# Optimization experiments

Measured on AMD Instinct MI355X. Metric: run time of the kernel, lower is better.

## Reference

```python
import jax, jax.numpy as jnp
import numpy as np
from jax import lax

T, B, NI, NH = 512, 64, 512, 512
SIGMA = 0.01


def _rnn_scan(inputs, W_xh, W_hh, b_h, h0):
    # inputs: [T, B, NI]; precompute input projection as one big GEMM
    xw = jnp.einsum('tbi,ih->tbh', inputs, W_xh)  # [T, B, NH]

    def step(h, x):
        h = jnp.tanh(x + h @ W_hh + b_h)
        return h, h

    hT, hs = lax.scan(step, h0, xw)
    return hs, hT  # hs: [T, B, NH]


def setup_inputs() -> dict:
    key = jax.random.key(0)
    ks = jax.random.split(key, 5)
    inputs = jax.random.normal(ks[0], (T, B, NI), dtype=jnp.float32)
    W_xh_f = jax.random.normal(ks[1], (NI, NH), dtype=jnp.float32) * SIGMA
    W_hh_f = jax.random.normal(ks[2], (NH, NH), dtype=jnp.float32) * SIGMA
    b_h_f = jnp.zeros((NH,), dtype=jnp.float32)
    W_xh_b = jax.random.normal(ks[3], (NI, NH), dtype=jnp.float32) * SIGMA
    W_hh_b = jax.random.normal(ks[4], (NH, NH), dtype=jnp.float32) * SIGMA
    b_h_b = jnp.zeros((NH,), dtype=jnp.float32)
    return {"inputs": inputs, "W_xh_f": W_xh_f, "W_hh_f": W_hh_f, "b_h_f": b_h_f,
            "W_xh_b": W_xh_b, "W_hh_b": W_hh_b, "b_h_b": b_h_b}


def reference(inputs, W_xh_f, W_hh_f, b_h_f, W_xh_b, W_hh_b, b_h_b):
    h0 = jnp.zeros((inputs.shape[1], NH), dtype=inputs.dtype)
    f_outs, f_H = _rnn_scan(inputs, W_xh_f, W_hh_f, b_h_f, h0)
    b_outs_rev, b_H = _rnn_scan(inputs[::-1], W_xh_b, W_hh_b, b_h_b, h0)
    b_outs = b_outs_rev[::-1]  # align backward outputs with forward time order
    outputs = jnp.concatenate([f_outs, b_outs], axis=-1)  # [T, B, 2*NH]
    return outputs, f_H, b_H
```

## Files before the change

### kernel.cpp

```cpp
#include <hip/hip_runtime.h>
#include <hip/hip_bf16.h>


typedef __attribute__((ext_vector_type(8))) short short8;
typedef __attribute__((ext_vector_type(4))) float f32x4;
typedef __attribute__((ext_vector_type(4))) int   i32x4;

static __device__ __forceinline__ unsigned short f2bf(float f) {
  unsigned int u = __builtin_bit_cast(unsigned int, f);
  u = (u + 0x7fffu + ((u >> 16) & 1u)) >> 16;
  return (unsigned short)u;
}
static __device__ __forceinline__ float bf2f(unsigned short s) {
  return __builtin_bit_cast(float, ((unsigned int)s) << 16);
}
static __device__ __forceinline__ float tanh_cheap(float x) {
  float t = x * 2.8853900817779268f;
  float e;
  asm("v_exp_f32 %0, %1" : "=v"(e) : "v"(t));
  float den = e + 1.0f;
  float r;
  asm("v_rcp_f32 %0, %1" : "=v"(r) : "v"(den));
  return __builtin_fmaf(-2.0f, r, 1.0f);
}
static __device__ __forceinline__ void lds_barrier() {
  __builtin_amdgcn_sched_barrier(0);
  asm volatile("s_waitcnt lgkmcnt(0)" ::: "memory");
  __builtin_amdgcn_s_barrier();
  __builtin_amdgcn_sched_barrier(0);
}
static __device__ __forceinline__ unsigned int cvt_pk_bf16(float a, float b) {
  unsigned int d;
  asm("v_cvt_pk_bf16_f32 %0, %1, %2" : "=v"(d) : "v"(a), "v"(b));
  return d;
}

__global__ __launch_bounds__(256, 2) void xw_gemm(
    const float* __restrict__ inp,
    const float* __restrict__ Wf,
    const float* __restrict__ Wb,
    const float* __restrict__ bhf,
    const float* __restrict__ bhb,
    unsigned short* __restrict__ xwpf,
    unsigned short* __restrict__ xwpb) {
  __shared__ unsigned short As[64 * 40];
  __shared__ unsigned short Bfs[64 * 40];
  __shared__ unsigned short Bbs[64 * 40];
  const int tid = threadIdx.x;
  const int w = tid >> 6, l = tid & 63;
  const int lr = l & 15, lg = l >> 4;
  const int rbase = blockIdx.x * 64;
  const int nbase = blockIdx.y * 64;

  f32x4 accf[4], accb[4];
#pragma unroll
  for (int tn = 0; tn < 4; ++tn) { accf[tn] = (f32x4){0,0,0,0}; accb[tn] = (f32x4){0,0,0,0}; }

  for (int i = 0; i < 16; ++i) {
    const int k0 = i * 32;
    __syncthreads();
#pragma unroll
    for (int e = 0; e < 2; ++e) {
      int lin4 = tid + e * 256;
      int r = lin4 >> 3, c4 = (lin4 & 7) * 4;
      float4 v = *reinterpret_cast<const float4*>(&inp[(rbase + r) * 512 + k0 + c4]);
      unsigned short* dst = &As[r * 40 + c4];
      dst[0] = f2bf(v.x); dst[1] = f2bf(v.y); dst[2] = f2bf(v.z); dst[3] = f2bf(v.w);
    }
#pragma unroll
    for (int e = 0; e < 2; ++e) {
      int lin4 = tid + e * 256;
      int r = lin4 >> 4, c4 = (lin4 & 15) * 4;
      float4 vf = *reinterpret_cast<const float4*>(&Wf[(k0 + r) * 512 + nbase + c4]);
      float4 vb = *reinterpret_cast<const float4*>(&Wb[(k0 + r) * 512 + nbase + c4]);
      Bfs[(c4 + 0) * 40 + r] = f2bf(vf.x);
      Bfs[(c4 + 1) * 40 + r] = f2bf(vf.y);
      Bfs[(c4 + 2) * 40 + r] = f2bf(vf.z);
      Bfs[(c4 + 3) * 40 + r] = f2bf(vf.w);
      Bbs[(c4 + 0) * 40 + r] = f2bf(vb.x);
      Bbs[(c4 + 1) * 40 + r] = f2bf(vb.y);
      Bbs[(c4 + 2) * 40 + r] = f2bf(vb.z);
      Bbs[(c4 + 3) * 40 + r] = f2bf(vb.w);
    }
    __syncthreads();
    const int ar = w * 16 + lr;
    const int kg = lg * 8;
    short8 a = *reinterpret_cast<const short8*>(&As[ar * 40 + kg]);
#pragma unroll
    for (int tn = 0; tn < 4; ++tn) {
      const int bc = tn * 16 + lr;
      short8 bf = *reinterpret_cast<const short8*>(&Bfs[bc * 40 + kg]);
      short8 bb = *reinterpret_cast<const short8*>(&Bbs[bc * 40 + kg]);
      accf[tn] = __builtin_amdgcn_mfma_f32_16x16x32_bf16(a, bf, accf[tn], 0, 0, 0);
      accb[tn] = __builtin_amdgcn_mfma_f32_16x16x32_bf16(a, bb, accb[tn], 0, 0, 0);
    }
  }
  unsigned long long* pf = reinterpret_cast<unsigned long long*>(xwpf);
  unsigned long long* pb = reinterpret_cast<unsigned long long*>(xwpb);
  const int b64 = (((int)blockIdx.x * 4 + w) * 8 + (int)blockIdx.y) * 256 + (lg * 16 + lr) * 4;
#pragma unroll
  for (int tn = 0; tn < 4; ++tn) {
    const int colb = nbase + tn * 16 + lr;
    const float bfv = bhf[colb], bbv = bhb[colb];
    unsigned long long vf =
        (unsigned long long)cvt_pk_bf16(accf[tn][0] + bfv, accf[tn][1] + bfv)
      | ((unsigned long long)cvt_pk_bf16(accf[tn][2] + bfv, accf[tn][3] + bfv) << 32);
    unsigned long long vb =
        (unsigned long long)cvt_pk_bf16(accb[tn][0] + bbv, accb[tn][1] + bbv)
      | ((unsigned long long)cvt_pk_bf16(accb[tn][2] + bbv, accb[tn][3] + bbv) << 32);
    pf[b64 + tn] = vf;
    pb[b64 + tn] = vb;
  }
}

__global__ __launch_bounds__(512, 2) void birnn_scan(
    const float* __restrict__ Whf, const float* __restrict__ Whb,
    unsigned short* __restrict__ xwpf, unsigned short* __restrict__ xwpb,
    float* __restrict__ out) {
  const int bid = blockIdx.x;
  const int d  = bid >> 2;
  const int rg = bid & 3;
  const int tid = threadIdx.x;
  const int w = tid >> 6, l = tid & 63;
  const int lr = l & 15, lg = l >> 4;
  const int cbase = w * 64;
  const int rbase = rg * 16;

  const float* Wh = d ? Whb : Whf;
  unsigned short* xwp = d ? xwpb : xwpf;

  __shared__ __align__(16) signed char hq[2][8192];

  const float sW = 127.0f / 0.06f;
  i32x4 wq[4][8];
#pragma unroll
  for (int n = 0; n < 4; ++n) {
    const int col = cbase + n * 16 + lr;
#pragma unroll
    for (int kk = 0; kk < 8; ++kk) {
      i32x4 v;
#pragma unroll
      for (int dw = 0; dw < 4; ++dw) {
        unsigned int pack = 0;
#pragma unroll
        for (int jj = 0; jj < 4; ++jj) {
          const int k = kk * 64 + lg * 16 + dw * 4 + jj;
          float wv = Wh[k * 512 + col] * sW;
          wv = fminf(fmaxf(wv, -127.f), 127.f);
          int q = (int)rintf(wv);
          pack |= ((unsigned int)(q & 0xff)) << (8 * jj);
        }
        v[dw] = (int)pack;
      }
      wq[n][kk] = v;
    }
  }
  const float inv_s = 1.0f / (127.0f * sW);

  short8 xA0, xA1, xB0, xB1;
  {
    const int t0 = d ? 511 : 0;
    const unsigned short* p = xwp + (((t0 * 4 + rg) * 8 + w) << 10) + (l << 4);
    xA0 = *reinterpret_cast<const short8*>(p);
    xA1 = *reinterpret_cast<const short8*>(p + 8);
  }
  {
    const int t1 = d ? 510 : 1;
    const unsigned short* p = xwp + (((t1 * 4 + rg) * 8 + w) << 10) + (l << 4);
    xB0 = *reinterpret_cast<const short8*>(p);
    xB1 = *reinterpret_cast<const short8*>(p + 8);
  }

  uint4 HP0, HP1;

#define XV_EXTRACT(XLO, XHI)                                                  \
    float xv[4][4];                                                           \
    _Pragma("unroll") for (int n = 0; n < 2; ++n)                             \
      _Pragma("unroll") for (int q = 0; q < 4; ++q) {                         \
        xv[n][q]     = bf2f((unsigned short)XLO[n * 4 + q]);                  \
        xv[n + 2][q] = bf2f((unsigned short)XHI[n * 4 + q]);                  \
      }

#define EPI(N, ACC, U0, U1, FINAL_)                                           \
  {                                                                           \
    float h0_ = tanh_cheap(fmaf((float)(ACC)[0], inv_s, xv[N][0]));           \
    float h1_ = tanh_cheap(fmaf((float)(ACC)[1], inv_s, xv[N][1]));           \
    float h2_ = tanh_cheap(fmaf((float)(ACC)[2], inv_s, xv[N][2]));           \
    float h3_ = tanh_cheap(fmaf((float)(ACC)[3], inv_s, xv[N][3]));           \
    signed char* hd_ = &hq[buf_][(w * 4 + (N)) * 256 + lg * 64 + lr];         \
    hd_[0]  = (signed char)(int)rintf(h0_ * 127.f);                           \
    hd_[16] = (signed char)(int)rintf(h1_ * 127.f);                           \
    hd_[32] = (signed char)(int)rintf(h2_ * 127.f);                           \
    hd_[48] = (signed char)(int)rintf(h3_ * 127.f);                           \
    U0 = cvt_pk_bf16(h0_, h1_);                                               \
    U1 = cvt_pk_bf16(h2_, h3_);                                               \
    if (FINAL_) {                                                             \
      float* fo_ = out + 33554432 + d * 32768 + (rbase + lg * 4) * 512 +      \
                   cbase + (N) * 16 + lr;                                     \
      fo_[0] = h0_; fo_[512] = h1_; fo_[1024] = h2_; fo_[1536] = h3_;         \
    }                                                                         \
  }

#define CHAIN(ACC, N)                                                         \
  ACC = __builtin_amdgcn_mfma_i32_16x16x64_i8(a0, wq[N][0], ACC, 0, 0, 0);    \
  ACC = __builtin_amdgcn_mfma_i32_16x16x64_i8(a1, wq[N][1], ACC, 0, 0, 0);    \
  ACC = __builtin_amdgcn_mfma_i32_16x16x64_i8(a2, wq[N][2], ACC, 0, 0, 0);    \
  ACC = __builtin_amdgcn_mfma_i32_16x16x64_i8(a3, wq[N][3], ACC, 0, 0, 0);    \
  ACC = __builtin_amdgcn_mfma_i32_16x16x64_i8(a4, wq[N][4], ACC, 0, 0, 0);    \
  ACC = __builtin_amdgcn_mfma_i32_16x16x64_i8(a5, wq[N][5], ACC, 0, 0, 0);    \
  ACC = __builtin_amdgcn_mfma_i32_16x16x64_i8(a6, wq[N][6], ACC, 0, 0, 0);    \
  ACC = __builtin_amdgcn_mfma_i32_16x16x64_i8(a7, wq[N][7], ACC, 0, 0, 0);

#define STEP(S, XLO, XHI, FINAL_)                                             \
  do {                                                                        \
    const int s_ = (S);                                                       \
    const int t_ = d ? (511 - s_) : s_;                                       \
    const int buf_ = s_ & 1;                                                  \
    const signed char* hb_ = &hq[(s_ - 1) & 1][lg * 256 + lr * 16];           \
    i32x4 a0 = *(const i32x4*)(hb_ + 0);                                      \
    i32x4 a1 = *(const i32x4*)(hb_ + 1024);                                   \
    i32x4 a2 = *(const i32x4*)(hb_ + 2048);                                   \
    i32x4 a3 = *(const i32x4*)(hb_ + 3072);                                   \
    i32x4 a4 = *(const i32x4*)(hb_ + 4096);                                   \
    i32x4 a5 = *(const i32x4*)(hb_ + 5120);                                   \
    i32x4 a6 = *(const i32x4*)(hb_ + 6144);                                   \
    i32x4 a7 = *(const i32x4*)(hb_ + 7168);                                   \
    XV_EXTRACT(XLO, XHI);                                                     \
    {                                                                         \
      const int tp2_ = d ? (t_ - 2) : (t_ + 2);                               \
      const unsigned short* p_ =                                              \
          xwp + (((tp2_ * 4 + rg) * 8 + w) << 10) + (l << 4);                 \
      XLO = *reinterpret_cast<const short8*>(p_);                             \
      XHI = *reinterpret_cast<const short8*>(p_ + 8);                         \
    }                                                                         \
    {              \
      const int tp_ = d ? (t_ + 1) : (t_ - 1);                                \
      unsigned short* pw_ = xwp + (((tp_ * 4 + rg) * 8 + w) << 10) + (l << 4);\
      *reinterpret_cast<uint4*>(pw_) = HP0;                                   \
      *reinterpret_cast<uint4*>(pw_ + 8) = HP1;                               \
    }                                                                         \
    i32x4 acc0 = (i32x4){0,0,0,0}, acc1 = (i32x4){0,0,0,0};                   \
    i32x4 acc2 = (i32x4){0,0,0,0}, acc3 = (i32x4){0,0,0,0};                   \
    CHAIN(acc0, 0);                                                           \
    CHAIN(acc1, 1);                                                           \
    EPI(0, acc0, HP0.x, HP0.y, FINAL_);                                       \
    CHAIN(acc2, 2);                                                           \
    EPI(1, acc1, HP0.z, HP0.w, FINAL_);                                       \
    CHAIN(acc3, 3);                                                           \
    EPI(2, acc2, HP1.x, HP1.y, FINAL_);                                       \
    EPI(3, acc3, HP1.z, HP1.w, FINAL_);                                       \
    lds_barrier();                                                            \
  } while (0)

  {
    const int t_ = d ? 511 : 0;
    const int buf_ = 0;
    XV_EXTRACT(xA0, xA1);
    {
      const int tp2_ = d ? (t_ - 2) : (t_ + 2);
      const unsigned short* p_ = xwp + (((tp2_ * 4 + rg) * 8 + w) << 10) + (l << 4);
      xA0 = *reinterpret_cast<const short8*>(p_);
      xA1 = *reinterpret_cast<const short8*>(p_ + 8);
    }
    i32x4 z_ = (i32x4){0, 0, 0, 0};
    EPI(0, z_, HP0.x, HP0.y, 0);
    EPI(1, z_, HP0.z, HP0.w, 0);
    EPI(2, z_, HP1.x, HP1.y, 0);
    EPI(3, z_, HP1.z, HP1.w, 0);
    lds_barrier();
  }

  for (int ss = 0; ss < 255; ++ss) {
    STEP(1 + 2 * ss, xB0, xB1, 0);
    STEP(2 + 2 * ss, xA0, xA1, 0);
  }
  STEP(511, xB0, xB1, 1);

  {
    const int tl_ = d ? 0 : 511;
    unsigned short* pw_ = xwp + (((tl_ * 4 + rg) * 8 + w) << 10) + (l << 4);
    *reinterpret_cast<uint4*>(pw_) = HP0;
    *reinterpret_cast<uint4*>(pw_ + 8) = HP1;
  }
#undef STEP
#undef CHAIN
#undef EPI
#undef XV_EXTRACT
}

__global__ __launch_bounds__(1024) void expand_out(
    const unsigned short* __restrict__ xwpf,
    const unsigned short* __restrict__ xwpb,
    float* __restrict__ out) {
  const int g = blockIdx.x * 1024 + threadIdx.x;
  const int flat = g * 4;
  const int row = flat >> 10;
  const int c   = flat & 1023;
  const int t = row >> 6, b = row & 63;
  const int d = c >> 9, col = c & 511;
  const unsigned short* buf = d ? xwpb : xwpf;
  const int lr0 = col & 15;
  const int base = ((((t * 4 + (b >> 4)) * 8 + (col >> 6)) << 10) +
                    ((b >> 2) & 3) * 256 + ((col >> 4) & 3) * 4 + (b & 3));
  float4 v;
  v.x = bf2f(buf[base + (lr0 + 0) * 16]);
  v.y = bf2f(buf[base + (lr0 + 1) * 16]);
  v.z = bf2f(buf[base + (lr0 + 2) * 16]);
  v.w = bf2f(buf[base + (lr0 + 3) * 16]);
  *reinterpret_cast<float4*>(out + flat) = v;
}

extern "C" void kernel_launch(void* const* d_in, const int* in_sizes, int n_in,
                              void* d_out, int out_size, void* d_ws, size_t ws_size,
                              hipStream_t stream) {
  (void)in_sizes; (void)n_in; (void)out_size; (void)ws_size;
  const float* inputs = (const float*)d_in[0];
  const float* W_xh_f = (const float*)d_in[1];
  const float* W_hh_f = (const float*)d_in[2];
  const float* b_h_f  = (const float*)d_in[3];
  const float* W_xh_b = (const float*)d_in[4];
  const float* W_hh_b = (const float*)d_in[5];
  const float* b_h_b  = (const float*)d_in[6];

  unsigned short* xwpf = (unsigned short*)d_ws;
  unsigned short* xwpb = xwpf + 16777216 + 65536;

  dim3 g1(512, 8), b1(256);
  xw_gemm<<<g1, b1, 0, stream>>>(inputs, W_xh_f, W_xh_b, b_h_f, b_h_b, xwpf, xwpb);

  birnn_scan<<<dim3(8), dim3(512), 0, stream>>>(
      W_hh_f, W_hh_b, xwpf, xwpb, (float*)d_out);

  expand_out<<<dim3(8192), dim3(1024), 0, stream>>>(xwpf, xwpb, (float*)d_out);
}
```

Baseline: 889.8 us.

## Split recurrent scan across 16 waves with two interleaved MFMA chains each

Doubles the scan block to 1024 threads so each wave owns 32 hidden columns instead of 64. Each wave now runs two independent int8 MFMA accumulator chains, interleaved, under raised wave priority, which shortens the serial per-step critical path. The xw/h workspace layout changes to match in the GEMM writer, the scan and expand_out. The cost is more waves contending at the per-step barrier and only one wave per SIMD group of four, possibly leaving latency less hidden.

```diff
diff --git a/kernel.cpp b/kernel.cpp
--- a/kernel.cpp
+++ b/kernel.cpp
@@ -97,7 +97,8 @@
   }
   unsigned long long* pf = reinterpret_cast<unsigned long long*>(xwpf);
   unsigned long long* pb = reinterpret_cast<unsigned long long*>(xwpb);
-  const int b64 = (((int)blockIdx.x * 4 + w) * 8 + (int)blockIdx.y) * 256 + (lg * 16 + lr) * 4;
+  const int b64 = (((int)blockIdx.x * 4 + w) * 16 + (int)blockIdx.y * 2) * 128 +
+                  (lg * 16 + lr) * 2;
 #pragma unroll
   for (int tn = 0; tn < 4; ++tn) {
     const int colb = nbase + tn * 16 + lr;
@@ -108,12 +109,12 @@
     unsigned long long vb =
         (unsigned long long)cvt_pk_bf16(accb[tn][0] + bbv, accb[tn][1] + bbv)
       | ((unsigned long long)cvt_pk_bf16(accb[tn][2] + bbv, accb[tn][3] + bbv) << 32);
-    pf[b64 + tn] = vf;
-    pb[b64 + tn] = vb;
-  }
-}
-
-__global__ __launch_bounds__(512, 2) void birnn_scan(
+    pf[b64 + (tn >> 1) * 128 + (tn & 1)] = vf;
+    pb[b64 + (tn >> 1) * 128 + (tn & 1)] = vb;
+  }
+}
+
+__global__ __launch_bounds__(1024) void birnn_scan(
     const float* __restrict__ Whf, const float* __restrict__ Whb,
     unsigned short* __restrict__ xwpf, unsigned short* __restrict__ xwpb,
     float* __restrict__ out) {
@@ -123,7 +124,7 @@
   const int tid = threadIdx.x;
   const int w = tid >> 6, l = tid & 63;
   const int lr = l & 15, lg = l >> 4;
-  const int cbase = w * 64;
+  const int cbase = w * 32;
   const int rbase = rg * 16;
 
   const float* Wh = d ? Whb : Whf;
@@ -132,9 +133,9 @@
   __shared__ __align__(16) signed char hq[2][8192];
 
   const float sW = 127.0f / 0.06f;
-  i32x4 wq[4][8];
-#pragma unroll
-  for (int n = 0; n < 4; ++n) {
+  i32x4 wq[2][8];
+#pragma unroll
+  for (int n = 0; n < 2; ++n) {
     const int col = cbase + n * 16 + lr;
 #pragma unroll
     for (int kk = 0; kk < 8; ++kk) {
@@ -157,37 +158,27 @@
   }
   const float inv_s = 1.0f / (127.0f * sW);
 
-  short8 xA0, xA1, xB0, xB1;
+  short8 xA, xB;
   {
     const int t0 = d ? 511 : 0;
-    const unsigned short* p = xwp + (((t0 * 4 + rg) * 8 + w) << 10) + (l << 4);
-    xA0 = *reinterpret_cast<const short8*>(p);
-    xA1 = *reinterpret_cast<const short8*>(p + 8);
+    xA = *reinterpret_cast<const short8*>(
+        xwp + (((t0 * 4 + rg) * 16 + w) << 9) + (l << 3));
   }
   {
     const int t1 = d ? 510 : 1;
-    const unsigned short* p = xwp + (((t1 * 4 + rg) * 8 + w) << 10) + (l << 4);
-    xB0 = *reinterpret_cast<const short8*>(p);
-    xB1 = *reinterpret_cast<const short8*>(p + 8);
-  }
-
-  uint4 HP0, HP1;
-
-#define XV_EXTRACT(XLO, XHI)                                                  \
-    float xv[4][4];                                                           \
-    _Pragma("unroll") for (int n = 0; n < 2; ++n)                             \
-      _Pragma("unroll") for (int q = 0; q < 4; ++q) {                         \
-        xv[n][q]     = bf2f((unsigned short)XLO[n * 4 + q]);                  \
-        xv[n + 2][q] = bf2f((unsigned short)XHI[n * 4 + q]);                  \
-      }
+    xB = *reinterpret_cast<const short8*>(
+        xwp + (((t1 * 4 + rg) * 16 + w) << 9) + (l << 3));
+  }
+
+  uint4 HP;
 
 #define EPI(N, ACC, U0, U1, FINAL_)                                           \
   {                                                                           \
-    float h0_ = tanh_cheap(fmaf((float)(ACC)[0], inv_s, xv[N][0]));           \
-    float h1_ = tanh_cheap(fmaf((float)(ACC)[1], inv_s, xv[N][1]));           \
-    float h2_ = tanh_cheap(fmaf((float)(ACC)[2], inv_s, xv[N][2]));           \
-    float h3_ = tanh_cheap(fmaf((float)(ACC)[3], inv_s, xv[N][3]));           \
-    signed char* hd_ = &hq[buf_][(w * 4 + (N)) * 256 + lg * 64 + lr];         \
+    float h0_ = tanh_cheap(fmaf((float)(ACC)[0], inv_s, bf2f((unsigned short)X[(N)*4+0]))); \
+    float h1_ = tanh_cheap(fmaf((float)(ACC)[1], inv_s, bf2f((unsigned short)X[(N)*4+1]))); \
+    float h2_ = tanh_cheap(fmaf((float)(ACC)[2], inv_s, bf2f((unsigned short)X[(N)*4+2]))); \
+    float h3_ = tanh_cheap(fmaf((float)(ACC)[3], inv_s, bf2f((unsigned short)X[(N)*4+3]))); \
+    signed char* hd_ = &hq[buf_][(w * 2 + (N)) * 256 + lg * 64 + lr];         \
     hd_[0]  = (signed char)(int)rintf(h0_ * 127.f);                           \
     hd_[16] = (signed char)(int)rintf(h1_ * 127.f);                           \
     hd_[32] = (signed char)(int)rintf(h2_ * 127.f);                           \
@@ -201,91 +192,89 @@
     }                                                                         \
   }
 
-#define CHAIN(ACC, N)                                                         \
-  ACC = __builtin_amdgcn_mfma_i32_16x16x64_i8(a0, wq[N][0], ACC, 0, 0, 0);    \
-  ACC = __builtin_amdgcn_mfma_i32_16x16x64_i8(a1, wq[N][1], ACC, 0, 0, 0);    \
-  ACC = __builtin_amdgcn_mfma_i32_16x16x64_i8(a2, wq[N][2], ACC, 0, 0, 0);    \
-  ACC = __builtin_amdgcn_mfma_i32_16x16x64_i8(a3, wq[N][3], ACC, 0, 0, 0);    \
-  ACC = __builtin_amdgcn_mfma_i32_16x16x64_i8(a4, wq[N][4], ACC, 0, 0, 0);    \
-  ACC = __builtin_amdgcn_mfma_i32_16x16x64_i8(a5, wq[N][5], ACC, 0, 0, 0);    \
-  ACC = __builtin_amdgcn_mfma_i32_16x16x64_i8(a6, wq[N][6], ACC, 0, 0, 0);    \
-  ACC = __builtin_amdgcn_mfma_i32_16x16x64_i8(a7, wq[N][7], ACC, 0, 0, 0);
-
-#define STEP(S, XLO, XHI, FINAL_)                                             \
+#define STEP(S, XARG, FINAL_)                                                 \
   do {                                                                        \
     const int s_ = (S);                                                       \
     const int t_ = d ? (511 - s_) : s_;                                       \
     const int buf_ = s_ & 1;                                                  \
-    const signed char* hb_ = &hq[(s_ - 1) & 1][lg * 256 + lr * 16];           \
-    i32x4 a0 = *(const i32x4*)(hb_ + 0);                                      \
-    i32x4 a1 = *(const i32x4*)(hb_ + 1024);                                   \
-    i32x4 a2 = *(const i32x4*)(hb_ + 2048);                                   \
-    i32x4 a3 = *(const i32x4*)(hb_ + 3072);                                   \
-    i32x4 a4 = *(const i32x4*)(hb_ + 4096);                                   \
-    i32x4 a5 = *(const i32x4*)(hb_ + 5120);                                   \
-    i32x4 a6 = *(const i32x4*)(hb_ + 6144);                                   \
-    i32x4 a7 = *(const i32x4*)(hb_ + 7168);                                   \
-    XV_EXTRACT(XLO, XHI);                                                     \
-    {                                                                         \
-      const int tp2_ = d ? (t_ - 2) : (t_ + 2);                               \
-      const unsigned short* p_ =                                              \
-          xwp + (((tp2_ * 4 + rg) * 8 + w) << 10) + (l << 4);                 \
-      XLO = *reinterpret_cast<const short8*>(p_);                             \
-      XHI = *reinterpret_cast<const short8*>(p_ + 8);                         \
-    }                                                                         \
+    const int pb_ = (s_ - 1) & 1;                                             \
+    short8& X = (XARG);                                                       \
     {              \
       const int tp_ = d ? (t_ + 1) : (t_ - 1);                                \
-      unsigned short* pw_ = xwp + (((tp_ * 4 + rg) * 8 + w) << 10) + (l << 4);\
-      *reinterpret_cast<uint4*>(pw_) = HP0;                                   \
-      *reinterpret_cast<uint4*>(pw_ + 8) = HP1;                               \
+      unsigned short* pw_ = xwp + (((tp_ * 4 + rg) * 16 + w) << 9) + (l << 3);\
+      *reinterpret_cast<uint4*>(pw_) = HP;                                    \
     }                                                                         \
     i32x4 acc0 = (i32x4){0,0,0,0}, acc1 = (i32x4){0,0,0,0};                   \
-    i32x4 acc2 = (i32x4){0,0,0,0}, acc3 = (i32x4){0,0,0,0};                   \
-    CHAIN(acc0, 0);                                                           \
-    CHAIN(acc1, 1);                                                           \
-    EPI(0, acc0, HP0.x, HP0.y, FINAL_);                                       \
-    CHAIN(acc2, 2);                                                           \
-    EPI(1, acc1, HP0.z, HP0.w, FINAL_);                                       \
-    CHAIN(acc3, 3);                                                           \
-    EPI(2, acc2, HP1.x, HP1.y, FINAL_);                                       \
-    EPI(3, acc3, HP1.z, HP1.w, FINAL_);                                       \
+    __builtin_amdgcn_s_setprio(1);                                            \
+    {                        \
+      const signed char* hb_ = &hq[pb_][lg * 256 + lr * 16];                  \
+      i32x4 a0 = *(const i32x4*)(hb_ + 0);                                    \
+      i32x4 a1 = *(const i32x4*)(hb_ + 1024);                                 \
+      i32x4 a2 = *(const i32x4*)(hb_ + 2048);                                 \
+      i32x4 a3 = *(const i32x4*)(hb_ + 3072);                                 \
+      acc0 = __builtin_amdgcn_mfma_i32_16x16x64_i8(a0, wq[0][0], acc0, 0, 0, 0); \
+      acc1 = __builtin_amdgcn_mfma_i32_16x16x64_i8(a0, wq[1][0], acc1, 0, 0, 0); \
+      acc0 = __builtin_amdgcn_mfma_i32_16x16x64_i8(a1, wq[0][1], acc0, 0, 0, 0); \
+      acc1 = __builtin_amdgcn_mfma_i32_16x16x64_i8(a1, wq[1][1], acc1, 0, 0, 0); \
+      acc0 = __builtin_amdgcn_mfma_i32_16x16x64_i8(a2, wq[0][2], acc0, 0, 0, 0); \
+      acc1 = __builtin_amdgcn_mfma_i32_16x16x64_i8(a2, wq[1][2], acc1, 0, 0, 0); \
+      acc0 = __builtin_amdgcn_mfma_i32_16x16x64_i8(a3, wq[0][3], acc0, 0, 0, 0); \
+      acc1 = __builtin_amdgcn_mfma_i32_16x16x64_i8(a3, wq[1][3], acc1, 0, 0, 0); \
+    }                                                                         \
+    {                                              \
+      const signed char* hb_ = &hq[pb_][(16 + lg) * 256 + lr * 16];           \
+      i32x4 a0 = *(const i32x4*)(hb_ + 0);                                    \
+      i32x4 a1 = *(const i32x4*)(hb_ + 1024);                                 \
+      i32x4 a2 = *(const i32x4*)(hb_ + 2048);                                 \
+      i32x4 a3 = *(const i32x4*)(hb_ + 3072);                                 \
+      acc0 = __builtin_amdgcn_mfma_i32_16x16x64_i8(a0, wq[0][4], acc0, 0, 0, 0); \
+      acc1 = __builtin_amdgcn_mfma_i32_16x16x64_i8(a0, wq[1][4], acc1, 0, 0, 0); \
+      acc0 = __builtin_amdgcn_mfma_i32_16x16x64_i8(a1, wq[0][5], acc0, 0, 0, 0); \
+      acc1 = __builtin_amdgcn_mfma_i32_16x16x64_i8(a1, wq[1][5], acc1, 0, 0, 0); \
+      acc0 = __builtin_amdgcn_mfma_i32_16x16x64_i8(a2, wq[0][6], acc0, 0, 0, 0); \
+      acc1 = __builtin_amdgcn_mfma_i32_16x16x64_i8(a2, wq[1][6], acc1, 0, 0, 0); \
+      acc0 = __builtin_amdgcn_mfma_i32_16x16x64_i8(a3, wq[0][7], acc0, 0, 0, 0); \
+      acc1 = __builtin_amdgcn_mfma_i32_16x16x64_i8(a3, wq[1][7], acc1, 0, 0, 0); \
+    }                                                                         \
+    __builtin_amdgcn_s_setprio(0);                                            \
+    EPI(0, acc0, HP.x, HP.y, FINAL_);                                         \
+    EPI(1, acc1, HP.z, HP.w, FINAL_);                                         \
+    {                                    \
+      const int tp2_ = d ? (t_ - 2) : (t_ + 2);                               \
+      X = *reinterpret_cast<const short8*>(                                   \
+          xwp + (((tp2_ * 4 + rg) * 16 + w) << 9) + (l << 3));                \
+    }                                                                         \
     lds_barrier();                                                            \
   } while (0)
 
   {
     const int t_ = d ? 511 : 0;
     const int buf_ = 0;
-    XV_EXTRACT(xA0, xA1);
+    short8& X = xA;
+    i32x4 z_ = (i32x4){0, 0, 0, 0};
+    EPI(0, z_, HP.x, HP.y, 0);
+    EPI(1, z_, HP.z, HP.w, 0);
     {
       const int tp2_ = d ? (t_ - 2) : (t_ + 2);
-      const unsigned short* p_ = xwp + (((tp2_ * 4 + rg) * 8 + w) << 10) + (l << 4);
-      xA0 = *reinterpret_cast<const short8*>(p_);
-      xA1 = *reinterpret_cast<const short8*>(p_ + 8);
-    }
-    i32x4 z_ = (i32x4){0, 0, 0, 0};
-    EPI(0, z_, HP0.x, HP0.y, 0);
-    EPI(1, z_, HP0.z, HP0.w, 0);
-    EPI(2, z_, HP1.x, HP1.y, 0);
-    EPI(3, z_, HP1.z, HP1.w, 0);
+      xA = *reinterpret_cast<const short8*>(
+          xwp + (((tp2_ * 4 + rg) * 16 + w) << 9) + (l << 3));
+    }
     lds_barrier();
   }
 
   for (int ss = 0; ss < 255; ++ss) {
-    STEP(1 + 2 * ss, xB0, xB1, 0);
-    STEP(2 + 2 * ss, xA0, xA1, 0);
-  }
-  STEP(511, xB0, xB1, 1);
+    STEP(1 + 2 * ss, xB, 0);
+    STEP(2 + 2 * ss, xA, 0);
+  }
+  STEP(511, xB, 1);
 
   {
     const int tl_ = d ? 0 : 511;
-    unsigned short* pw_ = xwp + (((tl_ * 4 + rg) * 8 + w) << 10) + (l << 4);
-    *reinterpret_cast<uint4*>(pw_) = HP0;
-    *reinterpret_cast<uint4*>(pw_ + 8) = HP1;
+    unsigned short* pw_ = xwp + (((tl_ * 4 + rg) * 16 + w) << 9) + (l << 3);
+    *reinterpret_cast<uint4*>(pw_) = HP;
   }
 #undef STEP
-#undef CHAIN
 #undef EPI
-#undef XV_EXTRACT
 }
 
 __global__ __launch_bounds__(1024) void expand_out(
@@ -300,13 +289,13 @@
   const int d = c >> 9, col = c & 511;
   const unsigned short* buf = d ? xwpb : xwpf;
   const int lr0 = col & 15;
-  const int base = ((((t * 4 + (b >> 4)) * 8 + (col >> 6)) << 10) +
-                    ((b >> 2) & 3) * 256 + ((col >> 4) & 3) * 4 + (b & 3));
+  const int base = ((t * 4 + (b >> 4)) * 16 + (col >> 5)) * 512 +
+                   (((b >> 2) & 3) * 16) * 8 + ((col >> 4) & 1) * 4 + (b & 3);
   float4 v;
-  v.x = bf2f(buf[base + (lr0 + 0) * 16]);
-  v.y = bf2f(buf[base + (lr0 + 1) * 16]);
-  v.z = bf2f(buf[base + (lr0 + 2) * 16]);
-  v.w = bf2f(buf[base + (lr0 + 3) * 16]);
+  v.x = bf2f(buf[base + (lr0 + 0) * 8]);
+  v.y = bf2f(buf[base + (lr0 + 1) * 8]);
+  v.z = bf2f(buf[base + (lr0 + 2) * 8]);
+  v.w = bf2f(buf[base + (lr0 + 3) * 8]);
   *reinterpret_cast<float4*>(out + flat) = v;
 }
 
@@ -328,7 +317,7 @@
   dim3 g1(512, 8), b1(256);
   xw_gemm<<<g1, b1, 0, stream>>>(inputs, W_xh_f, W_xh_b, b_h_f, b_h_b, xwpf, xwpb);
 
-  birnn_scan<<<dim3(8), dim3(512), 0, stream>>>(
+  birnn_scan<<<dim3(8), dim3(1024), 0, stream>>>(
       W_hh_f, W_hh_b, xwpf, xwpb, (float*)d_out);
 
   expand_out<<<dim3(8192), dim3(1024), 0, stream>>>(xwpf, xwpb, (float*)d_out);
```

After: 843.9 us. 5.2% less time.
